# Optimization experiments

Hardware: AMD Instinct MI355X
Metric: run time of the kernel (lower is better)

Reference implementation:

```python
import jax, jax.numpy as jnp
import numpy as np

TOP_K = 2

def setup_inputs() -> dict:
    key = jax.random.key(0)
    k1, k2 = jax.random.split(key)
    N, D, E = 16384, 2048, 64
    x = jax.random.normal(k1, (N, D), dtype=jnp.float32)
    W = jax.random.normal(k2, (D, E), dtype=jnp.float32) * (1.0 / np.sqrt(D))
    b = jnp.zeros((E,), dtype=jnp.float32)
    return {"x": x, "W": W, "b": b}

def reference(x, W, b):
    # gate linear: [N, D] @ [D, E] + [E]
    logits = jnp.einsum('nd,de->ne', x, W) + b
    gates = jax.nn.softmax(logits, axis=-1)
    topk_vals, topk_idx = jax.lax.top_k(gates, TOP_K)  # [N, k]
    N = gates.shape[0]
    rows = jnp.arange(N)[:, None]  # [N, 1] broadcast over k
    dispatch_mask = jnp.zeros_like(gates).at[rows, topk_idx].set(topk_vals)
    return dispatch_mask, topk_idx
```

## Files before the change

### kernel.cpp

```cpp
#include <hip/hip_runtime.h>
#include <math.h>

#define NROWS 16384
#define DDIM  2048
#define EEXP  64
#define RB    32
#define KC    64
#define NCH   (DDIM / KC)

#define WSPLIT_BYTES 786432
#define CHSTRIDE     24576

typedef short        bf16x8 __attribute__((ext_vector_type(8)));
typedef float        f32x16 __attribute__((ext_vector_type(16)));
typedef float        f32x4  __attribute__((ext_vector_type(4)));
typedef unsigned int u32x4  __attribute__((ext_vector_type(4)));

union V4 { u32x4 u; bf16x8 s; };

static __device__ __forceinline__ void split3x2(float f0, float f1,
                                                unsigned int &p0, unsigned int &p1,
                                                unsigned int &p2) {
    unsigned int a0 = __float_as_uint(f0), b0 = __float_as_uint(f1);
    unsigned int ah = a0 & 0xffff0000u,   bh = b0 & 0xffff0000u;
    float fa1 = f0 - __uint_as_float(ah);
    float fb1 = f1 - __uint_as_float(bh);
    unsigned int a1 = __float_as_uint(fa1), b1 = __float_as_uint(fb1);
    unsigned int am = a1 & 0xffff0000u,     bm = b1 & 0xffff0000u;
    float fa2 = fa1 - __uint_as_float(am);
    float fb2 = fb1 - __uint_as_float(bm);
    p0 = (a0 >> 16) | bh;
    p1 = (a1 >> 16) | bm;
    p2 = (__float_as_uint(fa2) >> 16) | (__float_as_uint(fb2) & 0xffff0000u);
}

static __device__ __forceinline__ void cvt8(f32x4 u, f32x4 v, V4 &q0, V4 &q1, V4 &q2) {
    unsigned int a, b, c;
    split3x2(u[0], u[1], a, b, c); q0.u[0] = a; q1.u[0] = b; q2.u[0] = c;
    split3x2(u[2], u[3], a, b, c); q0.u[1] = a; q1.u[1] = b; q2.u[1] = c;
    split3x2(v[0], v[1], a, b, c); q0.u[2] = a; q1.u[2] = b; q2.u[2] = c;
    split3x2(v[2], v[3], a, b, c); q0.u[3] = a; q1.u[3] = b; q2.u[3] = c;
}

#define MM(ACC, A, B) ACC = __builtin_amdgcn_mfma_f32_32x32x16_bf16((A), (B), ACC, 0, 0, 0)

#define STR_(x) #x
#define GLD(dst, voff, base, IMM)                                             \
    asm volatile("global_load_dwordx4 %0, %1, %2 offset:" STR_(IMM)           \
                 : "=v"(dst) : "v"(voff), "s"(base))
#define WAITV(N)                                                              \
    asm volatile("s_waitcnt vmcnt(" STR_(N) ")" ::: "memory");                \
    __builtin_amdgcn_sched_barrier(0)

#define CONSUME(XA, XB, B0, B1, B2) {                                         \
    V4 a0, a1, a2; cvt8(XA, XB, a0, a1, a2);                                  \
    MM(accA, a0.s, B0.s); MM(accB, a0.s, B1.s); MM(accA, a1.s, B0.s);         \
    MM(accB, a0.s, B2.s); MM(accA, a1.s, B1.s); MM(accB, a2.s, B0.s); }

#define ISSUE(XA, XB, B0, B1, B2, IMM0, IMM1)                                 \
    GLD(XA, voffx, x, IMM0); GLD(XB, voffx, x, IMM1);                         \
    GLD(B0.u, voffB, wsplit, 0); GLD(B1.u, voffB, wsplit, 16);                \
    GLD(B2.u, voffB, wsplit, 32); voffB += CHSTRIDE;

#define STEP(N, XA, XB, B0, B1, B2, IMM0, IMM1)                               \
    WAITV(N); CONSUME(XA, XB, B0, B1, B2) ISSUE(XA, XB, B0, B1, B2, IMM0, IMM1)

#define DRAIN(N, XA, XB, B0, B1, B2)                                          \
    WAITV(N); CONSUME(XA, XB, B0, B1, B2)

__global__ __launch_bounds__(256)
void wsplit_kernel(const float* __restrict__ W, unsigned char* __restrict__ ws) {
    const int t  = blockIdx.x * 256 + threadIdx.x;
    const int e  = t & 63;
    const int ko = t >> 6;
    const int k0 = ko * 8;
    f32x4 u, v;
#pragma unroll
    for (int j = 0; j < 4; ++j) u[j] = W[(size_t)(k0 + j) * EEXP + e];
#pragma unroll
    for (int j = 0; j < 4; ++j) v[j] = W[(size_t)(k0 + 4 + j) * EEXP + e];
    V4 q0, q1, q2;
    cvt8(u, v, q0, q1, q2);
    const int c  = k0 >> 6;
    const int kg = (k0 >> 4) & 3;
    const int h  = (k0 >> 3) & 1;
    const int et = e >> 5;
    const int ln = h * 32 + (e & 31);
    unsigned char* d = ws + (size_t)(((((c * 4 + kg) * 2 + et) * 64) + ln) * 48);
    *(u32x4*)(d +  0) = q0.u;
    *(u32x4*)(d + 16) = q1.u;
    *(u32x4*)(d + 32) = q2.u;
}

__global__ __launch_bounds__(512, 2)
void router_kernel(const float* __restrict__ x,
                   const unsigned char* __restrict__ wsplit,
                   const float* __restrict__ bias_v,
                   float* __restrict__ mask_out,
                   float* __restrict__ idx_out) {
    __shared__ __align__(16) float ep[8192];

    const int tid  = threadIdx.x;
    const int lane = tid & 63;
    const int w    = __builtin_amdgcn_readfirstlane(tid >> 6);
    const int kg   = w & 3;
    const int et   = w >> 2;
    const int row0 = blockIdx.x * RB;
    const int l31  = lane & 31;
    const int h    = lane >> 5;

    unsigned int voffx = (unsigned int)(((row0 + l31) * DDIM + kg * 16 + h * 8) * 4);
    unsigned int voffB = (unsigned int)(((kg * 2 + et) * 64 + lane) * 48);

    f32x16 accA, accB;
#pragma unroll
    for (int i = 0; i < 16; ++i) { accA[i] = 0.f; accB[i] = 0.f; }

    f32x4 X0a, X0b, X1a, X1b, X2a, X2b, X3a, X3b;
    f32x4 X4a, X4b, X5a, X5b, X6a, X6b, X7a, X7b;
    V4 B00, B01, B02, B10, B11, B12, B20, B21, B22, B30, B31, B32;
    V4 B40, B41, B42, B50, B51, B52, B60, B61, B62, B70, B71, B72;

    ISSUE(X0a, X0b, B00, B01, B02,    0,   16)
    ISSUE(X1a, X1b, B10, B11, B12,  256,  272)
    ISSUE(X2a, X2b, B20, B21, B22,  512,  528)
    ISSUE(X3a, X3b, B30, B31, B32,  768,  784)
    ISSUE(X4a, X4b, B40, B41, B42, 1024, 1040)
    ISSUE(X5a, X5b, B50, B51, B52, 1280, 1296)
    ISSUE(X6a, X6b, B60, B61, B62, 1536, 1552)
    ISSUE(X7a, X7b, B70, B71, B72, 1792, 1808)
    voffx += 2048;

#pragma unroll 1
    for (int j = 0; j < 3; ++j) {
        STEP(35, X0a, X0b, B00, B01, B02,    0,   16)
        STEP(35, X1a, X1b, B10, B11, B12,  256,  272)
        STEP(35, X2a, X2b, B20, B21, B22,  512,  528)
        STEP(35, X3a, X3b, B30, B31, B32,  768,  784)
        STEP(35, X4a, X4b, B40, B41, B42, 1024, 1040)
        STEP(35, X5a, X5b, B50, B51, B52, 1280, 1296)
        STEP(35, X6a, X6b, B60, B61, B62, 1536, 1552)
        STEP(35, X7a, X7b, B70, B71, B72, 1792, 1808)
        voffx += 2048;
    }

    DRAIN(35, X0a, X0b, B00, B01, B02)
    DRAIN(30, X1a, X1b, B10, B11, B12)
    DRAIN(25, X2a, X2b, B20, B21, B22)
    DRAIN(20, X3a, X3b, B30, B31, B32)
    DRAIN(15, X4a, X4b, B40, B41, B42)
    DRAIN(10, X5a, X5b, B50, B51, B52)
    DRAIN(5,  X6a, X6b, B60, B61, B62)
    DRAIN(0,  X7a, X7b, B70, B71, B72)

#pragma unroll
    for (int r = 0; r < 16; ++r) {
        const int rowl = (r & 3) + 8 * (r >> 2) + 4 * h;
        ep[kg * 2048 + rowl * 64 + et * 32 + l31] = accA[r] + accB[r];
    }
    __syncthreads();

    const float bias = bias_v[lane];
#pragma unroll
    for (int rr = 0; rr < 4; ++rr) {
        const int rl  = w * 4 + rr;
        const int row = row0 + rl;
        float logit = bias + ep[rl * 64 + lane]
                           + ep[2048 + rl * 64 + lane]
                           + ep[4096 + rl * 64 + lane]
                           + ep[6144 + rl * 64 + lane];

        float m = logit;
#pragma unroll
        for (int off = 32; off >= 1; off >>= 1) m = fmaxf(m, __shfl_xor(m, off));
        float ex = __expf(logit - m);
        float s = ex;
#pragma unroll
        for (int off = 32; off >= 1; off >>= 1) s += __shfl_xor(s, off);
        float gate = ex / s;

        float v1 = logit; int i1 = lane;
#pragma unroll
        for (int off = 32; off >= 1; off >>= 1) {
            float ov = __shfl_xor(v1, off);
            int   oi = __shfl_xor(i1, off);
            if (ov > v1 || (ov == v1 && oi < i1)) { v1 = ov; i1 = oi; }
        }
        float v2 = (lane == i1) ? -INFINITY : logit; int i2 = lane;
#pragma unroll
        for (int off = 32; off >= 1; off >>= 1) {
            float ov = __shfl_xor(v2, off);
            int   oi = __shfl_xor(i2, off);
            if (ov > v2 || (ov == v2 && oi < i2)) { v2 = ov; i2 = oi; }
        }

        float outv = (lane == i1 || lane == i2) ? gate : 0.0f;
        mask_out[(size_t)row * EEXP + lane] = outv;
        if (lane == 0) {
            idx_out[row * 2 + 0] = (float)i1;
            idx_out[row * 2 + 1] = (float)i2;
        }
    }
}

extern "C" void kernel_launch(void* const* d_in, const int* in_sizes, int n_in,
                              void* d_out, int out_size, void* d_ws, size_t ws_size,
                              hipStream_t stream) {
    const float* x = (const float*)d_in[0];
    const float* W = (const float*)d_in[1];
    const float* b = (const float*)d_in[2];
    float* mask_out = (float*)d_out;
    float* idx_out  = mask_out + (size_t)NROWS * EEXP;
    unsigned char* ws = (unsigned char*)d_ws;

    wsplit_kernel<<<dim3(64), dim3(256), 0, stream>>>(W, ws);
    router_kernel<<<dim3(NROWS / RB), dim3(512), 0, stream>>>(x, ws, b, mask_out, idx_out);
}
```

Before: 241.7 us.

## Stage x tiles through swizzled double-buffered LDS with coalesced row loads

Replaces the per-lane strided global loads of x (inline-asm deep register pipeline) with fully coalesced row-wise loads into an XOR-swizzled, double-buffered shared-memory tile, from which each wave reads its MFMA fragments. The W split fragments are now loaded directly per chunk without prefetch. It also remaps block indices with a swizzle across the grid. The aim is better DRAM coalescing for x, at the cost of an LDS round trip, a barrier per stage, less latency hiding for W loads and a larger LDS footprint that may limit occupancy.

```diff
diff --git a/kernel.cpp b/kernel.cpp
--- a/kernel.cpp
+++ b/kernel.cpp
@@ -5,11 +5,8 @@
 #define DDIM  2048
 #define EEXP  64
 #define RB    32
-#define KC    64
-#define NCH   (DDIM / KC)
-
-#define WSPLIT_BYTES 786432
-#define CHSTRIDE     24576
+#define NST   8
+#define CHSTRIDE 24576
 
 typedef short        bf16x8 __attribute__((ext_vector_type(8)));
 typedef float        f32x16 __attribute__((ext_vector_type(16)));
@@ -44,30 +41,6 @@
 
 #define MM(ACC, A, B) ACC = __builtin_amdgcn_mfma_f32_32x32x16_bf16((A), (B), ACC, 0, 0, 0)
 
-#define STR_(x) #x
-#define GLD(dst, voff, base, IMM)                                             \
-    asm volatile("global_load_dwordx4 %0, %1, %2 offset:" STR_(IMM)           \
-                 : "=v"(dst) : "v"(voff), "s"(base))
-#define WAITV(N)                                                              \
-    asm volatile("s_waitcnt vmcnt(" STR_(N) ")" ::: "memory");                \
-    __builtin_amdgcn_sched_barrier(0)
-
-#define CONSUME(XA, XB, B0, B1, B2) {                                         \
-    V4 a0, a1, a2; cvt8(XA, XB, a0, a1, a2);                                  \
-    MM(accA, a0.s, B0.s); MM(accB, a0.s, B1.s); MM(accA, a1.s, B0.s);         \
-    MM(accB, a0.s, B2.s); MM(accA, a1.s, B1.s); MM(accB, a2.s, B0.s); }
-
-#define ISSUE(XA, XB, B0, B1, B2, IMM0, IMM1)                                 \
-    GLD(XA, voffx, x, IMM0); GLD(XB, voffx, x, IMM1);                         \
-    GLD(B0.u, voffB, wsplit, 0); GLD(B1.u, voffB, wsplit, 16);                \
-    GLD(B2.u, voffB, wsplit, 32); voffB += CHSTRIDE;
-
-#define STEP(N, XA, XB, B0, B1, B2, IMM0, IMM1)                               \
-    WAITV(N); CONSUME(XA, XB, B0, B1, B2) ISSUE(XA, XB, B0, B1, B2, IMM0, IMM1)
-
-#define DRAIN(N, XA, XB, B0, B1, B2)                                          \
-    WAITV(N); CONSUME(XA, XB, B0, B1, B2)
-
 __global__ __launch_bounds__(256)
 void wsplit_kernel(const float* __restrict__ W, unsigned char* __restrict__ ws) {
     const int t  = blockIdx.x * 256 + threadIdx.x;
@@ -98,61 +71,82 @@
                    const float* __restrict__ bias_v,
                    float* __restrict__ mask_out,
                    float* __restrict__ idx_out) {
-    __shared__ __align__(16) float ep[8192];
+    __shared__ __align__(16) float smem[16384];
 
     const int tid  = threadIdx.x;
     const int lane = tid & 63;
     const int w    = __builtin_amdgcn_readfirstlane(tid >> 6);
     const int kg   = w & 3;
     const int et   = w >> 2;
-    const int row0 = blockIdx.x * RB;
     const int l31  = lane & 31;
     const int h    = lane >> 5;
 
-    unsigned int voffx = (unsigned int)(((row0 + l31) * DDIM + kg * 16 + h * 8) * 4);
-    unsigned int voffB = (unsigned int)(((kg * 2 + et) * 64 + lane) * 48);
+    const int bid  = blockIdx.x;
+    const int bswz = (bid & 7) * ((int)gridDim.x >> 3) + (bid >> 3);
+    const int row0 = bswz * RB;
+
+    const int srow = 4 * w;
+
+    const unsigned char* wp = wsplit + (size_t)(((kg * 2 + et) * 64 + lane) * 48);
 
     f32x16 accA, accB;
 #pragma unroll
     for (int i = 0; i < 16; ++i) { accA[i] = 0.f; accB[i] = 0.f; }
 
-    f32x4 X0a, X0b, X1a, X1b, X2a, X2b, X3a, X3b;
-    f32x4 X4a, X4b, X5a, X5b, X6a, X6b, X7a, X7b;
-    V4 B00, B01, B02, B10, B11, B12, B20, B21, B22, B30, B31, B32;
-    V4 B40, B41, B42, B50, B51, B52, B60, B61, B62, B70, B71, B72;
-
-    ISSUE(X0a, X0b, B00, B01, B02,    0,   16)
-    ISSUE(X1a, X1b, B10, B11, B12,  256,  272)
-    ISSUE(X2a, X2b, B20, B21, B22,  512,  528)
-    ISSUE(X3a, X3b, B30, B31, B32,  768,  784)
-    ISSUE(X4a, X4b, B40, B41, B42, 1024, 1040)
-    ISSUE(X5a, X5b, B50, B51, B52, 1280, 1296)
-    ISSUE(X6a, X6b, B60, B61, B62, 1536, 1552)
-    ISSUE(X7a, X7b, B70, B71, B72, 1792, 1808)
-    voffx += 2048;
+    {
+        f32x4 X0, X1, X2, X3;
+        X0 = *(const f32x4*)(x + (size_t)(row0 + srow + 0) * DDIM + lane * 4);
+        X1 = *(const f32x4*)(x + (size_t)(row0 + srow + 1) * DDIM + lane * 4);
+        X2 = *(const f32x4*)(x + (size_t)(row0 + srow + 2) * DDIM + lane * 4);
+        X3 = *(const f32x4*)(x + (size_t)(row0 + srow + 3) * DDIM + lane * 4);
+#define XWR(I, V, B)                                                          \
+        *(f32x4*)(smem + (B) * 8192 + (srow + I) * 256 +                      \
+                  ((lane ^ ((srow + I) & 7)) << 2)) = V;
+        XWR(0, X0, 0) XWR(1, X1, 0) XWR(2, X2, 0) XWR(3, X3, 0)
+    }
+    __syncthreads();
 
 #pragma unroll 1
-    for (int j = 0; j < 3; ++j) {
-        STEP(35, X0a, X0b, B00, B01, B02,    0,   16)
-        STEP(35, X1a, X1b, B10, B11, B12,  256,  272)
-        STEP(35, X2a, X2b, B20, B21, B22,  512,  528)
-        STEP(35, X3a, X3b, B30, B31, B32,  768,  784)
-        STEP(35, X4a, X4b, B40, B41, B42, 1024, 1040)
-        STEP(35, X5a, X5b, B50, B51, B52, 1280, 1296)
-        STEP(35, X6a, X6b, B60, B61, B62, 1536, 1552)
-        STEP(35, X7a, X7b, B70, B71, B72, 1792, 1808)
-        voffx += 2048;
-    }
-
-    DRAIN(35, X0a, X0b, B00, B01, B02)
-    DRAIN(30, X1a, X1b, B10, B11, B12)
-    DRAIN(25, X2a, X2b, B20, B21, B22)
-    DRAIN(20, X3a, X3b, B30, B31, B32)
-    DRAIN(15, X4a, X4b, B40, B41, B42)
-    DRAIN(10, X5a, X5b, B50, B51, B52)
-    DRAIN(5,  X6a, X6b, B60, B61, B62)
-    DRAIN(0,  X7a, X7b, B70, B71, B72)
-
+    for (int s = 0; s < NST; ++s) {
+        const int  buf  = s & 1;
+        const bool more = (s + 1) < NST;
+
+        f32x4 X0, X1, X2, X3;
+        if (more) {
+            const float* xs = x + (size_t)(s + 1) * 256 + lane * 4;
+            X0 = *(const f32x4*)(xs + (size_t)(row0 + srow + 0) * DDIM);
+            X1 = *(const f32x4*)(xs + (size_t)(row0 + srow + 1) * DDIM);
+            X2 = *(const f32x4*)(xs + (size_t)(row0 + srow + 2) * DDIM);
+            X3 = *(const f32x4*)(xs + (size_t)(row0 + srow + 3) * DDIM);
+        }
+
+        const float* xb = smem + buf * 8192 + l31 * 256;
+        const int xr = l31 & 7;
+#pragma unroll
+        for (int cc = 0; cc < 4; ++cc) {
+            const int k0 = cc * 64 + kg * 16 + h * 8;
+            const int bb = k0 >> 2;
+            f32x4 lo = *(const f32x4*)(xb + (((bb    ) ^ xr) << 2));
+            f32x4 hi = *(const f32x4*)(xb + (((bb + 1) ^ xr) << 2));
+            const unsigned char* q = wp + (size_t)(s * 4 + cc) * CHSTRIDE;
+            V4 b0, b1, b2;
+            b0.u = *(const u32x4*)(q);
+            b1.u = *(const u32x4*)(q + 16);
+            b2.u = *(const u32x4*)(q + 32);
+            V4 a0, a1, a2;
+            cvt8(lo, hi, a0, a1, a2);
+            MM(accA, a0.s, b0.s); MM(accB, a0.s, b1.s); MM(accA, a1.s, b0.s);
+            MM(accB, a0.s, b2.s); MM(accA, a1.s, b1.s); MM(accB, a2.s, b0.s);
+        }
+
+        if (more) {
+            const int nb = buf ^ 1;
+            XWR(0, X0, nb) XWR(1, X1, nb) XWR(2, X2, nb) XWR(3, X3, nb)
+        }
+        __syncthreads();
+    }
+
+    float* ep = smem;
 #pragma unroll
     for (int r = 0; r < 16; ++r) {
         const int rowl = (r & 3) + 8 * (r >> 2) + 4 * h;
```

Measured after the change: 212.3 us. 12.2% less time.
